# Optimization experiments

Measured on AMD Instinct MI355X. Metric: run time of the kernel, lower is better.

## Reference

```python
import jax, jax.numpy as jnp
import numpy as np

B, S, D, H, V = 32, 1024, 512, 4, 8185
DH = 3 * D // H  # 384 per-head projection; q/k/v each 128
FFN = 4 * D
LN_EPS = 1e-3  # keras LayerNormalization default epsilon


def _pos_encoding(seq_len, d_model):
    pos = np.arange(seq_len)[:, None].astype(np.float32)
    i = np.arange(d_model)[None, :].astype(np.float32)
    angles = pos / np.power(10000.0, 2.0 * (i // 2) / np.float32(d_model))
    angles[:, 0::2] = np.sin(angles[:, 0::2])
    angles[:, 1::2] = np.cos(angles[:, 1::2])
    return jnp.asarray(angles, dtype=jnp.float32)  # [S, D]


def _layernorm(x, g, b):
    mu = jnp.mean(x, axis=-1, keepdims=True)
    var = jnp.mean(jnp.square(x - mu), axis=-1, keepdims=True)
    return (x - mu) * jax.lax.rsqrt(var + LN_EPS) * g + b


def setup_inputs() -> dict:
    key = jax.random.key(0)
    ks = jax.random.split(key, 8)
    sc = 0.02
    return {
        "inputs": jax.random.randint(ks[0], (B, S), 0, V, dtype=jnp.int32),
        "emb": jax.random.normal(ks[1], (V, D), jnp.float32) * sc,
        "Wp": jax.random.normal(ks[2], (H, D, DH), jnp.float32) * sc,
        "bp": jnp.zeros((H, DH), jnp.float32),
        "Wo": jax.random.normal(ks[3], (D, D), jnp.float32) * sc,
        "bo": jnp.zeros((D,), jnp.float32),
        "ln1_g": jnp.ones((D,), jnp.float32),
        "ln1_b": jnp.zeros((D,), jnp.float32),
        "W1": jax.random.normal(ks[4], (D, FFN), jnp.float32) * sc,
        "b1": jnp.zeros((FFN,), jnp.float32),
        "W2": jax.random.normal(ks[5], (FFN, D), jnp.float32) * sc,
        "b2": jnp.zeros((D,), jnp.float32),
        "ln2_g": jnp.ones((D,), jnp.float32),
        "ln2_b": jnp.zeros((D,), jnp.float32),
        "Wh": jax.random.normal(ks[6], (D, D), jnp.float32) * sc,
        "bh": jnp.zeros((D,), jnp.float32),
        "Wf": jax.random.normal(ks[7], (D, 1), jnp.float32) * sc,
        "bf": jnp.zeros((1,), jnp.float32),
    }


def reference(inputs, emb, Wp, bp, Wo, bo, ln1_g, ln1_b, W1, b1, W2, b2,
              ln2_g, ln2_b, Wh, bh, Wf, bf):
    b, s = inputs.shape
    x = emb[inputs] + _pos_encoding(s, emb.shape[1])[None]  # [B,S,D]

    # decoder block: batched per-head projections (q|k|v packed along last axis)
    res = x
    d = jnp.einsum('bsd,hde->bhse', x, Wp) + bp[:, None, :]  # [B,H,S,3*dh]
    q, k, v = jnp.split(d, 3, axis=-1)  # each [B,H,S,dh]
    # NOTE: source scales by rsqrt(seq_len) (tf.shape(k)[1]), not head dim
    scale = jax.lax.rsqrt(jnp.float32(s))
    scores = jnp.einsum('bhse,bhte->bhst', q, k) * scale  # [B,H,S,S]
    heads = jnp.einsum('bhst,bhte->bhse', scores, v)  # linear attn (no softmax)
    concat = heads.transpose(0, 2, 1, 3).reshape(b, s, -1)  # [B,S,D]
    attn = concat @ Wo + bo
    x = _layernorm(attn + res, ln1_g, ln1_b)
    h = jax.nn.relu(x @ W1 + b1) @ W2 + b2
    x = _layernorm(h + x, ln2_g, ln2_b)

    # classification head on first token
    x0 = x[:, 0]
    hid = jax.nn.relu(x0 @ Wh + bh)
    logits = hid @ Wf + bf  # [B,1]
    return logits, jax.nn.sigmoid(logits)
```

## Files before the change

### kernel.cpp

```cpp
#include <hip/hip_runtime.h>
#include <hip/hip_bf16.h>

__global__ __launch_bounds__(256) void qr_k(
    const int* __restrict__ inp, const float* __restrict__ emb,
    const float* __restrict__ Wp, const float* __restrict__ bp,
    float* __restrict__ X0, float* __restrict__ r, float* __restrict__ alpha,
    float* __restrict__ Acc, int* __restrict__ Cnt)
{
    __shared__ float xs[512];
    __shared__ float red[256];
    __shared__ float q0s[128];
    int b = blockIdx.x, h = blockIdx.y, t = threadIdx.x;
    if (b == 0 && h == 0) {
        if (t < 32) Acc[t] = 0.f;
        else if (t < 64) Cnt[t - 32] = 0;
    }
    int tok0 = inp[b * 1024];
#pragma unroll
    for (int rep = 0; rep < 2; rep++) {
        int d = t + rep * 256;
        float v = emb[(long)tok0 * 512 + d] + ((d & 1) ? 1.0f : 0.0f);
        xs[d] = v;
        if (h == 0) X0[b * 512 + d] = v;
    }
    __syncthreads();

    int f = t & 127, dh = t >> 7;
    const float* wq = Wp + (long)h * 196608 + f;
    float acc = 0.f;
#pragma unroll 8
    for (int d = dh * 256; d < dh * 256 + 256; d++)
        acc += xs[d] * wq[(long)d * 384];
    red[t] = acc;
    __syncthreads();
    if (t < 128) q0s[t] = red[t] + red[t + 128] + bp[h * 384 + t];
    __syncthreads();
    if (t < 128) red[t] = q0s[t] * bp[h * 384 + 128 + t];
    __syncthreads();
    for (int w = 64; w >= 1; w >>= 1) {
        if (t < w) red[t] += red[t + w];
        __syncthreads();
    }
    if (t == 0) alpha[b * 4 + h] = red[0];

    const float4* q4 = (const float4*)q0s;
#pragma unroll
    for (int rep = 0; rep < 2; rep++) {
        int d = t + rep * 256;
        const float4* wr = (const float4*)(Wp + ((long)(h * 512 + d)) * 384 + 128);
        float a2 = 0.f;
#pragma unroll 8
        for (int f4 = 0; f4 < 32; f4++) {
            float4 w = wr[f4], qq = q4[f4];
            a2 += w.x * qq.x + w.y * qq.y + w.z * qq.z + w.w * qq.w;
        }
        r[((long)(b * 4 + h)) * 512 + d] = a2;
    }
}

__global__ __launch_bounds__(256) void xu_k(
    const int* __restrict__ inp, const float* __restrict__ emb,
    const float* __restrict__ r, const float* __restrict__ alpha,
    float* __restrict__ Tpp, float* __restrict__ Gp)
{
    __shared__ float redT[4][4][64][8];
    __shared__ float redG[4][4];
    int b = blockIdx.x, sg = blockIdx.y, t = threadIdx.x;
    int wave = t >> 6, lane = t & 63;

    float rsv[4][8];
    float al[4];
#pragma unroll
    for (int h = 0; h < 4; h++) {
        const float4* rp = (const float4*)&r[((long)(b * 4 + h)) * 512 + lane * 8];
        float4 r0 = rp[0], r1 = rp[1];
        rsv[h][0] = r0.x; rsv[h][1] = r0.y; rsv[h][2] = r0.z; rsv[h][3] = r0.w;
        rsv[h][4] = r1.x; rsv[h][5] = r1.y; rsv[h][6] = r1.z; rsv[h][7] = r1.w;
        al[h] = alpha[b * 4 + h];
    }
    float w4[4];
#pragma unroll
    for (int j = 0; j < 4; j++) {
        float expo = (float)(lane * 8 + j * 2) * (1.0f / 512.0f);
        w4[j] = exp2f(-expo * 13.287712379549449f);
    }

    float accT[4][8] = {};
    float gacc[4] = {};
    int s0 = sg * 64 + wave * 16;
#pragma unroll
    for (int g = 0; g < 4; g++) {
        float xv[4][8];
        float up[4][4];
#pragma unroll
        for (int i = 0; i < 4; i++) {
            int srow = s0 + g * 4 + i;
            int tok = inp[b * 1024 + srow];
            const float4* e = (const float4*)&emb[(long)tok * 512 + lane * 8];
            float4 e0 = e[0], e1 = e[1];
            float sf = (float)srow;
            float sv[4], cv[4];
#pragma unroll
            for (int j = 0; j < 4; j++) {
                float ang = sf * w4[j];
                sv[j] = __sinf(ang);
                cv[j] = __cosf(ang);
            }
            xv[i][0] = e0.x + sv[0]; xv[i][1] = e0.y + cv[0];
            xv[i][2] = e0.z + sv[1]; xv[i][3] = e0.w + cv[1];
            xv[i][4] = e1.x + sv[2]; xv[i][5] = e1.y + cv[2];
            xv[i][6] = e1.z + sv[3]; xv[i][7] = e1.w + cv[3];
#pragma unroll
            for (int h = 0; h < 4; h++) {
                float acc = 0.f;
#pragma unroll
                for (int jj = 0; jj < 8; jj++) acc += xv[i][jj] * rsv[h][jj];
                up[i][h] = acc;
            }
        }
#pragma unroll
        for (int off = 32; off; off >>= 1) {
#pragma unroll
            for (int i = 0; i < 4; i++)
#pragma unroll
                for (int h = 0; h < 4; h++)
                    up[i][h] += __shfl_xor(up[i][h], off);
        }
#pragma unroll
        for (int i = 0; i < 4; i++) {
#pragma unroll
            for (int h = 0; h < 4; h++) {
                float u = up[i][h] + al[h];
                gacc[h] += u;
#pragma unroll
                for (int jj = 0; jj < 8; jj++) accT[h][jj] += u * xv[i][jj];
            }
        }
    }
#pragma unroll
    for (int h = 0; h < 4; h++) {
        *(float4*)&redT[wave][h][lane][0] =
            make_float4(accT[h][0], accT[h][1], accT[h][2], accT[h][3]);
        *(float4*)&redT[wave][h][lane][4] =
            make_float4(accT[h][4], accT[h][5], accT[h][6], accT[h][7]);
    }
    if (lane == 0) {
#pragma unroll
        for (int h = 0; h < 4; h++) redG[wave][h] = gacc[h];
    }
    __syncthreads();
    long base = (long)(b * 16 + sg) * 2048;
#pragma unroll
    for (int k = 0; k < 8; k++) {
        int idx = t + k * 256;
        int h = idx >> 9, d = idx & 511;
        float v = redT[0][h][d >> 3][d & 7] + redT[1][h][d >> 3][d & 7]
                + redT[2][h][d >> 3][d & 7] + redT[3][h][d >> 3][d & 7];
        Tpp[base + idx] = v;
    }
    if (t < 4) Gp[(b * 16 + sg) * 4 + t] =
        redG[0][t] + redG[1][t] + redG[2][t] + redG[3][t];
}

__global__ __launch_bounds__(256) void att1_k(
    const float* __restrict__ Tpp, const float* __restrict__ Gp,
    const float* __restrict__ Wp, const float* __restrict__ bp,
    float* __restrict__ C0)
{
    __shared__ float tps[512];
    __shared__ float red[256];
    int b = blockIdx.x, jt = blockIdx.y, t = threadIdx.x;
    int h = jt >> 1, e0 = (jt & 1) * 64;
#pragma unroll
    for (int i = 0; i < 2; i++) {
        int d = t + i * 256;
        float v = 0.f;
#pragma unroll 8
        for (int sg = 0; sg < 16; sg++)
            v += Tpp[(long)b * 32768 + sg * 2048 + h * 512 + d];
        tps[d] = v;
    }
    __syncthreads();
    int e = e0 + (t & 63), rg = t >> 6;
    const float* wv = Wp + (long)h * 196608 + 256 + e;
    float acc = 0.f;
#pragma unroll 8
    for (int d = rg * 128; d < rg * 128 + 128; d++)
        acc += tps[d] * wv[(long)d * 384];
    red[t] = acc;
    __syncthreads();
    if (t < 64) {
        float gam = 0.f;
#pragma unroll
        for (int sg = 0; sg < 16; sg++) gam += Gp[(b * 16 + sg) * 4 + h];
        float sum = red[t] + red[t + 64] + red[t + 128] + red[t + 192];
        float c = 0.03125f * (sum + gam * bp[h * 384 + 256 + e0 + t]);
        C0[b * 512 + h * 128 + e0 + t] = c;
    }
}

__global__ __launch_bounds__(256) void att2s_k(
    const float* __restrict__ C0, const float* __restrict__ Wo,
    const float* __restrict__ bo, const float* __restrict__ X0,
    float* __restrict__ A1, float* __restrict__ Stat)
{
    __shared__ float c0s[512];
    __shared__ float red[256];
    int b = blockIdx.x, jt = blockIdx.y, t = threadIdx.x;
    c0s[t] = C0[b * 512 + t];
    c0s[t + 256] = C0[b * 512 + t + 256];
    __syncthreads();
    int j = jt * 64 + (t & 63), rg = t >> 6;
    float acc = 0.f;
#pragma unroll 8
    for (int d = rg * 128; d < rg * 128 + 128; d++)
        acc += c0s[d] * Wo[(long)d * 512 + j];
    red[t] = acc;
    __syncthreads();
    if (t < 64) {
        int jj = jt * 64 + t;
        float a = red[t] + red[t + 64] + red[t + 128] + red[t + 192]
                + bo[jj] + X0[b * 512 + jj];
        A1[b * 512 + jj] = a;
        float s = a, q = a * a;
#pragma unroll
        for (int off = 32; off; off >>= 1) {
            s += __shfl_down(s, off);
            q += __shfl_down(q, off);
        }
        if (t == 0) {
            Stat[(b * 8 + jt) * 2]     = s;
            Stat[(b * 8 + jt) * 2 + 1] = q;
        }
    }
}

__global__ __launch_bounds__(256) void ffn1_k(
    const float* __restrict__ A1, const float* __restrict__ Stat,
    const float* __restrict__ g1, const float* __restrict__ b1v,
    const float* __restrict__ W1, float* __restrict__ Hp1)
{
    __shared__ float at[32][32];
    __shared__ float mrs[32][2];
    int jt = blockIdx.x, ks = blockIdx.y, t = threadIdx.x;
    if (t < 32) {
        float s = 0.f, q = 0.f;
#pragma unroll
        for (int p8 = 0; p8 < 8; p8++) {
            s += Stat[(t * 8 + p8) * 2];
            q += Stat[(t * 8 + p8) * 2 + 1];
        }
        float mean = s * (1.0f / 512.0f);
        float var = q * (1.0f / 512.0f) - mean * mean;
        mrs[t][0] = mean;
        mrs[t][1] = rsqrtf(var + 0.001f);
    }
    __syncthreads();
    {
        int row = t >> 3, f4 = t & 7;
        int col = ks * 32 + f4 * 4;
        float4 a4 = *(const float4*)&A1[(long)row * 512 + col];
        float4 g4 = *(const float4*)&g1[col];
        float4 bb = *(const float4*)&b1v[col];
        float mean = mrs[row][0], rstd = mrs[row][1];
        float4 v;
        v.x = (a4.x - mean) * rstd * g4.x + bb.x;
        v.y = (a4.y - mean) * rstd * g4.y + bb.y;
        v.z = (a4.z - mean) * rstd * g4.z + bb.z;
        v.w = (a4.w - mean) * rstd * g4.w + bb.w;
        ((float4*)at)[t] = v;
    }
    __syncthreads();
    int j = jt * 64 + (t & 63), rg = t >> 6;
    float acc[8] = {};
    const float* wp = W1 + (long)(ks * 32) * 2048 + j;
#pragma unroll 8
    for (int k = 0; k < 32; k++) {
        float wv = wp[(long)k * 2048];
#pragma unroll
        for (int rr = 0; rr < 8; rr++)
            acc[rr] += at[rg * 8 + rr][k] * wv;
    }
#pragma unroll
    for (int rr = 0; rr < 8; rr++)
        Hp1[((long)(ks * 32 + rg * 8 + rr)) * 2048 + j] = acc[rr];
}

__global__ __launch_bounds__(256) void ffn2_k(
    const float* __restrict__ Hp1, const float* __restrict__ b1,
    const float* __restrict__ W2, float* __restrict__ Hp2)
{
    __shared__ float at[32][32];
    int jt = blockIdx.x, ks2 = blockIdx.y, t = threadIdx.x;
    {
        int row = t >> 3, f4 = t & 7;
        int col4 = ks2 * 8 + f4;
        float4 v = ((const float4*)b1)[col4];
#pragma unroll
        for (int p = 0; p < 16; p++) {
            float4 pv = ((const float4*)Hp1)[(long)p * 16384 + row * 512 + col4];
            v.x += pv.x; v.y += pv.y; v.z += pv.z; v.w += pv.w;
        }
        v.x = fmaxf(v.x, 0.f); v.y = fmaxf(v.y, 0.f);
        v.z = fmaxf(v.z, 0.f); v.w = fmaxf(v.w, 0.f);
        ((float4*)at)[t] = v;
    }
    __syncthreads();
    int j = jt * 64 + (t & 63), rg = t >> 6;
    float acc[8] = {};
    const float* wp = W2 + (long)(ks2 * 32) * 512 + j;
#pragma unroll 8
    for (int k = 0; k < 32; k++) {
        float wv = wp[(long)k * 512];
#pragma unroll
        for (int rr = 0; rr < 8; rr++)
            acc[rr] += at[rg * 8 + rr][k] * wv;
    }
#pragma unroll
    for (int rr = 0; rr < 8; rr++)
        Hp2[((long)(ks2 * 32 + rg * 8 + rr)) * 512 + j] = acc[rr];
}

__global__ __launch_bounds__(256) void headp3_k(
    const float* __restrict__ Hp2, const float* __restrict__ b2,
    const float* __restrict__ A1, const float* __restrict__ Stat,
    const float* __restrict__ g1v, const float* __restrict__ b1v,
    const float* __restrict__ g2v, const float* __restrict__ b2v,
    const float* __restrict__ Wh, const float* __restrict__ bh,
    const float* __restrict__ Wf, const float* __restrict__ bf,
    float* __restrict__ Acc, int* __restrict__ Cnt, float* __restrict__ out)
{
    __shared__ float xs[512];
    __shared__ float red[256];
    __shared__ float sd[8];
    __shared__ float mr[2];
    int b = blockIdx.x, jt = blockIdx.y, t = threadIdx.x;
    if (t == 0) {
        float s = 0.f, q = 0.f;
#pragma unroll
        for (int p8 = 0; p8 < 8; p8++) {
            s += Stat[(b * 8 + p8) * 2];
            q += Stat[(b * 8 + p8) * 2 + 1];
        }
        float mean = s * (1.0f / 512.0f);
        mr[0] = mean;
        mr[1] = rsqrtf(q * (1.0f / 512.0f) - mean * mean + 0.001f);
    }
    __syncthreads();
    float mean1 = mr[0], rstd1 = mr[1];
    float a[2];
#pragma unroll
    for (int rep = 0; rep < 2; rep++) {
        int j = t + rep * 256;
        float y1 = (A1[b * 512 + j] - mean1) * rstd1 * g1v[j] + b1v[j];
        float v = b2[j] + y1;
#pragma unroll 16
        for (int ks = 0; ks < 64; ks++)
            v += Hp2[((long)(ks * 32 + b)) * 512 + j];
        a[rep] = v;
    }
    float s = a[0] + a[1];
#pragma unroll
    for (int off = 32; off; off >>= 1) s += __shfl_down(s, off);
    if ((t & 63) == 0) sd[t >> 6] = s;
    __syncthreads();
    float mean = (sd[0] + sd[1] + sd[2] + sd[3]) * (1.0f / 512.0f);
    float d0 = a[0] - mean, d1 = a[1] - mean;
    float v2 = d0 * d0 + d1 * d1;
#pragma unroll
    for (int off = 32; off; off >>= 1) v2 += __shfl_down(v2, off);
    if ((t & 63) == 0) sd[4 + (t >> 6)] = v2;
    __syncthreads();
    float var = (sd[4] + sd[5] + sd[6] + sd[7]) * (1.0f / 512.0f);
    float rstd = rsqrtf(var + 0.001f);
    xs[t] = d0 * rstd * g2v[t] + b2v[t];
    xs[t + 256] = d1 * rstd * g2v[t + 256] + b2v[t + 256];
    __syncthreads();

    int j = jt * 64 + (t & 63), rg = t >> 6;
    const float* w = Wh + j;
    float acc = 0.f;
#pragma unroll 8
    for (int d = rg * 128; d < rg * 128 + 128; d++)
        acc += xs[d] * w[(long)d * 512];
    red[t] = acc;
    __syncthreads();
    if (t < 64) {
        int jj = jt * 64 + t;
        float hid = red[t] + red[t + 64] + red[t + 128] + red[t + 192] + bh[jj];
        hid = fmaxf(hid, 0.f);
        float p = hid * Wf[jj];
#pragma unroll
        for (int off = 32; off; off >>= 1) p += __shfl_down(p, off);
        if (t == 0) {
            atomicAdd(&Acc[b], p);
            __threadfence();
            int old = atomicAdd(&Cnt[b], 1);
            if (old == 7) {
                float tot = atomicAdd(&Acc[b], 0.0f);
                float logit = tot + bf[0];
                out[b] = logit;
                out[32 + b] = 1.f / (1.f + expf(-logit));
            }
        }
    }
}

extern "C" void kernel_launch(void* const* d_in, const int* in_sizes, int n_in,
                              void* d_out, int out_size, void* d_ws, size_t ws_size,
                              hipStream_t stream)
{
    const int*   inputs = (const int*)  d_in[0];
    const float* emb    = (const float*)d_in[1];
    const float* Wp     = (const float*)d_in[2];
    const float* bp     = (const float*)d_in[3];
    const float* Wo     = (const float*)d_in[4];
    const float* bo     = (const float*)d_in[5];
    const float* ln1_g  = (const float*)d_in[6];
    const float* ln1_b  = (const float*)d_in[7];
    const float* W1     = (const float*)d_in[8];
    const float* b1     = (const float*)d_in[9];
    const float* W2     = (const float*)d_in[10];
    const float* b2     = (const float*)d_in[11];
    const float* ln2_g  = (const float*)d_in[12];
    const float* ln2_b  = (const float*)d_in[13];
    const float* Wh     = (const float*)d_in[14];
    const float* bh     = (const float*)d_in[15];
    const float* Wf     = (const float*)d_in[16];
    const float* bf     = (const float*)d_in[17];
    float* out = (float*)d_out;

    char* p = (char*)d_ws;
    float* X0    = (float*)p;  p += 65536;
    float* r     = (float*)p;  p += 262144;
    float* alpha = (float*)p;  p += 1024;
    float* Gp    = (float*)p;  p += 8192;
    float* Tpp   = (float*)p;  p += 4194304;
    float* C0    = (float*)p;  p += 65536;
    float* A1    = (float*)p;  p += 65536;
    float* Stat  = (float*)p;  p += 2048;
    float* Acc   = (float*)p;  p += 512;
    int*   Cnt   = (int*)p;    p += 512;
    float* Hp1   = (float*)p;  p += 4194304;
    float* Hp2   = (float*)p;  p += 4194304;

    qr_k<<<dim3(32, 4), 256, 0, stream>>>(inputs, emb, Wp, bp, X0, r, alpha,
                                          Acc, Cnt);
    xu_k<<<dim3(32, 16), 256, 0, stream>>>(inputs, emb, r, alpha, Tpp, Gp);
    att1_k<<<dim3(32, 8), 256, 0, stream>>>(Tpp, Gp, Wp, bp, C0);
    att2s_k<<<dim3(32, 8), 256, 0, stream>>>(C0, Wo, bo, X0, A1, Stat);
    ffn1_k<<<dim3(32, 16), 256, 0, stream>>>(A1, Stat, ln1_g, ln1_b, W1, Hp1);
    ffn2_k<<<dim3(8, 64), 256, 0, stream>>>(Hp1, b1, W2, Hp2);
    headp3_k<<<dim3(32, 8), 256, 0, stream>>>(Hp2, b2, A1, Stat,
                                              ln1_g, ln1_b, ln2_g, ln2_b,
                                              Wh, bh, Wf, bf, Acc, Cnt, out);
}
```

Baseline: 187.0 us.

## Fuse seven stage kernels into one persistent kernel with global atomic barriers

Replaces the chain of seven kernel launches with a single grid-stride persistent kernel of 512 blocks. Stages are separated by a software grid barrier built on atomic counters, and a small init kernel resets the counters. The aim is to remove per-launch gaps and tail effects between the small dependent stages. The barrier spins on atomics and assumes all 512 blocks are co-resident (launch bounds 256,2), so it risks deadlock if they are not, and it adds polling overhead.

```diff
diff --git a/kernel.cpp b/kernel.cpp
--- a/kernel.cpp
+++ b/kernel.cpp
@@ -1,406 +1,429 @@
 #include <hip/hip_runtime.h>
 #include <hip/hip_bf16.h>
 
-__global__ __launch_bounds__(256) void qr_k(
+__device__ __forceinline__ void gbar(int* __restrict__ bar, int nblk)
+{
+    __syncthreads();
+    __threadfence();
+    if (threadIdx.x == 0) {
+        atomicAdd(bar, 1);
+        while (atomicAdd(bar, 0) < nblk)
+            __builtin_amdgcn_s_sleep(1);
+    }
+    __syncthreads();
+    __threadfence();
+}
+
+__global__ __launch_bounds__(64) void init_k(
+    float* __restrict__ Acc, int* __restrict__ Cnt, int* __restrict__ Bar)
+{
+    int t = threadIdx.x;
+    if (t < 32) { Acc[t] = 0.f; Cnt[t] = 0; }
+    if (t < 8)  Bar[t] = 0;
+}
+
+__global__ __launch_bounds__(256, 2) void mega_k(
     const int* __restrict__ inp, const float* __restrict__ emb,
     const float* __restrict__ Wp, const float* __restrict__ bp,
-    float* __restrict__ X0, float* __restrict__ r, float* __restrict__ alpha,
-    float* __restrict__ Acc, int* __restrict__ Cnt)
-{
-    __shared__ float xs[512];
-    __shared__ float red[256];
-    __shared__ float q0s[128];
-    int b = blockIdx.x, h = blockIdx.y, t = threadIdx.x;
-    if (b == 0 && h == 0) {
-        if (t < 32) Acc[t] = 0.f;
-        else if (t < 64) Cnt[t - 32] = 0;
-    }
-    int tok0 = inp[b * 1024];
-#pragma unroll
-    for (int rep = 0; rep < 2; rep++) {
-        int d = t + rep * 256;
-        float v = emb[(long)tok0 * 512 + d] + ((d & 1) ? 1.0f : 0.0f);
-        xs[d] = v;
-        if (h == 0) X0[b * 512 + d] = v;
-    }
-    __syncthreads();
-
-    int f = t & 127, dh = t >> 7;
-    const float* wq = Wp + (long)h * 196608 + f;
-    float acc = 0.f;
-#pragma unroll 8
-    for (int d = dh * 256; d < dh * 256 + 256; d++)
-        acc += xs[d] * wq[(long)d * 384];
-    red[t] = acc;
-    __syncthreads();
-    if (t < 128) q0s[t] = red[t] + red[t + 128] + bp[h * 384 + t];
-    __syncthreads();
-    if (t < 128) red[t] = q0s[t] * bp[h * 384 + 128 + t];
-    __syncthreads();
-    for (int w = 64; w >= 1; w >>= 1) {
-        if (t < w) red[t] += red[t + w];
-        __syncthreads();
-    }
-    if (t == 0) alpha[b * 4 + h] = red[0];
-
-    const float4* q4 = (const float4*)q0s;
-#pragma unroll
-    for (int rep = 0; rep < 2; rep++) {
-        int d = t + rep * 256;
-        const float4* wr = (const float4*)(Wp + ((long)(h * 512 + d)) * 384 + 128);
-        float a2 = 0.f;
-#pragma unroll 8
-        for (int f4 = 0; f4 < 32; f4++) {
-            float4 w = wr[f4], qq = q4[f4];
-            a2 += w.x * qq.x + w.y * qq.y + w.z * qq.z + w.w * qq.w;
-        }
-        r[((long)(b * 4 + h)) * 512 + d] = a2;
-    }
-}
-
-__global__ __launch_bounds__(256) void xu_k(
-    const int* __restrict__ inp, const float* __restrict__ emb,
-    const float* __restrict__ r, const float* __restrict__ alpha,
-    float* __restrict__ Tpp, float* __restrict__ Gp)
-{
-    __shared__ float redT[4][4][64][8];
-    __shared__ float redG[4][4];
-    int b = blockIdx.x, sg = blockIdx.y, t = threadIdx.x;
-    int wave = t >> 6, lane = t & 63;
-
-    float rsv[4][8];
-    float al[4];
-#pragma unroll
-    for (int h = 0; h < 4; h++) {
-        const float4* rp = (const float4*)&r[((long)(b * 4 + h)) * 512 + lane * 8];
-        float4 r0 = rp[0], r1 = rp[1];
-        rsv[h][0] = r0.x; rsv[h][1] = r0.y; rsv[h][2] = r0.z; rsv[h][3] = r0.w;
-        rsv[h][4] = r1.x; rsv[h][5] = r1.y; rsv[h][6] = r1.z; rsv[h][7] = r1.w;
-        al[h] = alpha[b * 4 + h];
-    }
-    float w4[4];
-#pragma unroll
-    for (int j = 0; j < 4; j++) {
-        float expo = (float)(lane * 8 + j * 2) * (1.0f / 512.0f);
-        w4[j] = exp2f(-expo * 13.287712379549449f);
-    }
-
-    float accT[4][8] = {};
-    float gacc[4] = {};
-    int s0 = sg * 64 + wave * 16;
-#pragma unroll
-    for (int g = 0; g < 4; g++) {
-        float xv[4][8];
-        float up[4][4];
-#pragma unroll
-        for (int i = 0; i < 4; i++) {
-            int srow = s0 + g * 4 + i;
-            int tok = inp[b * 1024 + srow];
-            const float4* e = (const float4*)&emb[(long)tok * 512 + lane * 8];
-            float4 e0 = e[0], e1 = e[1];
-            float sf = (float)srow;
-            float sv[4], cv[4];
-#pragma unroll
-            for (int j = 0; j < 4; j++) {
-                float ang = sf * w4[j];
-                sv[j] = __sinf(ang);
-                cv[j] = __cosf(ang);
-            }
-            xv[i][0] = e0.x + sv[0]; xv[i][1] = e0.y + cv[0];
-            xv[i][2] = e0.z + sv[1]; xv[i][3] = e0.w + cv[1];
-            xv[i][4] = e1.x + sv[2]; xv[i][5] = e1.y + cv[2];
-            xv[i][6] = e1.z + sv[3]; xv[i][7] = e1.w + cv[3];
-#pragma unroll
-            for (int h = 0; h < 4; h++) {
-                float acc = 0.f;
-#pragma unroll
-                for (int jj = 0; jj < 8; jj++) acc += xv[i][jj] * rsv[h][jj];
-                up[i][h] = acc;
-            }
-        }
-#pragma unroll
-        for (int off = 32; off; off >>= 1) {
-#pragma unroll
-            for (int i = 0; i < 4; i++)
-#pragma unroll
-                for (int h = 0; h < 4; h++)
-                    up[i][h] += __shfl_xor(up[i][h], off);
-        }
-#pragma unroll
-        for (int i = 0; i < 4; i++) {
-#pragma unroll
-            for (int h = 0; h < 4; h++) {
-                float u = up[i][h] + al[h];
-                gacc[h] += u;
-#pragma unroll
-                for (int jj = 0; jj < 8; jj++) accT[h][jj] += u * xv[i][jj];
-            }
-        }
-    }
-#pragma unroll
-    for (int h = 0; h < 4; h++) {
-        *(float4*)&redT[wave][h][lane][0] =
-            make_float4(accT[h][0], accT[h][1], accT[h][2], accT[h][3]);
-        *(float4*)&redT[wave][h][lane][4] =
-            make_float4(accT[h][4], accT[h][5], accT[h][6], accT[h][7]);
-    }
-    if (lane == 0) {
-#pragma unroll
-        for (int h = 0; h < 4; h++) redG[wave][h] = gacc[h];
-    }
-    __syncthreads();
-    long base = (long)(b * 16 + sg) * 2048;
-#pragma unroll
-    for (int k = 0; k < 8; k++) {
-        int idx = t + k * 256;
-        int h = idx >> 9, d = idx & 511;
-        float v = redT[0][h][d >> 3][d & 7] + redT[1][h][d >> 3][d & 7]
-                + redT[2][h][d >> 3][d & 7] + redT[3][h][d >> 3][d & 7];
-        Tpp[base + idx] = v;
-    }
-    if (t < 4) Gp[(b * 16 + sg) * 4 + t] =
-        redG[0][t] + redG[1][t] + redG[2][t] + redG[3][t];
-}
-
-__global__ __launch_bounds__(256) void att1_k(
-    const float* __restrict__ Tpp, const float* __restrict__ Gp,
-    const float* __restrict__ Wp, const float* __restrict__ bp,
-    float* __restrict__ C0)
-{
-    __shared__ float tps[512];
-    __shared__ float red[256];
-    int b = blockIdx.x, jt = blockIdx.y, t = threadIdx.x;
-    int h = jt >> 1, e0 = (jt & 1) * 64;
-#pragma unroll
-    for (int i = 0; i < 2; i++) {
-        int d = t + i * 256;
-        float v = 0.f;
-#pragma unroll 8
-        for (int sg = 0; sg < 16; sg++)
-            v += Tpp[(long)b * 32768 + sg * 2048 + h * 512 + d];
-        tps[d] = v;
-    }
-    __syncthreads();
-    int e = e0 + (t & 63), rg = t >> 6;
-    const float* wv = Wp + (long)h * 196608 + 256 + e;
-    float acc = 0.f;
-#pragma unroll 8
-    for (int d = rg * 128; d < rg * 128 + 128; d++)
-        acc += tps[d] * wv[(long)d * 384];
-    red[t] = acc;
-    __syncthreads();
-    if (t < 64) {
-        float gam = 0.f;
-#pragma unroll
-        for (int sg = 0; sg < 16; sg++) gam += Gp[(b * 16 + sg) * 4 + h];
-        float sum = red[t] + red[t + 64] + red[t + 128] + red[t + 192];
-        float c = 0.03125f * (sum + gam * bp[h * 384 + 256 + e0 + t]);
-        C0[b * 512 + h * 128 + e0 + t] = c;
-    }
-}
-
-__global__ __launch_bounds__(256) void att2s_k(
-    const float* __restrict__ C0, const float* __restrict__ Wo,
-    const float* __restrict__ bo, const float* __restrict__ X0,
-    float* __restrict__ A1, float* __restrict__ Stat)
-{
-    __shared__ float c0s[512];
-    __shared__ float red[256];
-    int b = blockIdx.x, jt = blockIdx.y, t = threadIdx.x;
-    c0s[t] = C0[b * 512 + t];
-    c0s[t + 256] = C0[b * 512 + t + 256];
-    __syncthreads();
-    int j = jt * 64 + (t & 63), rg = t >> 6;
-    float acc = 0.f;
-#pragma unroll 8
-    for (int d = rg * 128; d < rg * 128 + 128; d++)
-        acc += c0s[d] * Wo[(long)d * 512 + j];
-    red[t] = acc;
-    __syncthreads();
-    if (t < 64) {
-        int jj = jt * 64 + t;
-        float a = red[t] + red[t + 64] + red[t + 128] + red[t + 192]
-                + bo[jj] + X0[b * 512 + jj];
-        A1[b * 512 + jj] = a;
-        float s = a, q = a * a;
-#pragma unroll
-        for (int off = 32; off; off >>= 1) {
-            s += __shfl_down(s, off);
-            q += __shfl_down(q, off);
-        }
-        if (t == 0) {
-            Stat[(b * 8 + jt) * 2]     = s;
-            Stat[(b * 8 + jt) * 2 + 1] = q;
-        }
-    }
-}
-
-__global__ __launch_bounds__(256) void ffn1_k(
-    const float* __restrict__ A1, const float* __restrict__ Stat,
-    const float* __restrict__ g1, const float* __restrict__ b1v,
-    const float* __restrict__ W1, float* __restrict__ Hp1)
-{
-    __shared__ float at[32][32];
-    __shared__ float mrs[32][2];
-    int jt = blockIdx.x, ks = blockIdx.y, t = threadIdx.x;
-    if (t < 32) {
-        float s = 0.f, q = 0.f;
-#pragma unroll
-        for (int p8 = 0; p8 < 8; p8++) {
-            s += Stat[(t * 8 + p8) * 2];
-            q += Stat[(t * 8 + p8) * 2 + 1];
-        }
-        float mean = s * (1.0f / 512.0f);
-        float var = q * (1.0f / 512.0f) - mean * mean;
-        mrs[t][0] = mean;
-        mrs[t][1] = rsqrtf(var + 0.001f);
-    }
-    __syncthreads();
-    {
-        int row = t >> 3, f4 = t & 7;
-        int col = ks * 32 + f4 * 4;
-        float4 a4 = *(const float4*)&A1[(long)row * 512 + col];
-        float4 g4 = *(const float4*)&g1[col];
-        float4 bb = *(const float4*)&b1v[col];
-        float mean = mrs[row][0], rstd = mrs[row][1];
-        float4 v;
-        v.x = (a4.x - mean) * rstd * g4.x + bb.x;
-        v.y = (a4.y - mean) * rstd * g4.y + bb.y;
-        v.z = (a4.z - mean) * rstd * g4.z + bb.z;
-        v.w = (a4.w - mean) * rstd * g4.w + bb.w;
-        ((float4*)at)[t] = v;
-    }
-    __syncthreads();
-    int j = jt * 64 + (t & 63), rg = t >> 6;
-    float acc[8] = {};
-    const float* wp = W1 + (long)(ks * 32) * 2048 + j;
-#pragma unroll 8
-    for (int k = 0; k < 32; k++) {
-        float wv = wp[(long)k * 2048];
-#pragma unroll
-        for (int rr = 0; rr < 8; rr++)
-            acc[rr] += at[rg * 8 + rr][k] * wv;
-    }
-#pragma unroll
-    for (int rr = 0; rr < 8; rr++)
-        Hp1[((long)(ks * 32 + rg * 8 + rr)) * 2048 + j] = acc[rr];
-}
-
-__global__ __launch_bounds__(256) void ffn2_k(
-    const float* __restrict__ Hp1, const float* __restrict__ b1,
-    const float* __restrict__ W2, float* __restrict__ Hp2)
-{
-    __shared__ float at[32][32];
-    int jt = blockIdx.x, ks2 = blockIdx.y, t = threadIdx.x;
-    {
-        int row = t >> 3, f4 = t & 7;
-        int col4 = ks2 * 8 + f4;
-        float4 v = ((const float4*)b1)[col4];
-#pragma unroll
-        for (int p = 0; p < 16; p++) {
-            float4 pv = ((const float4*)Hp1)[(long)p * 16384 + row * 512 + col4];
-            v.x += pv.x; v.y += pv.y; v.z += pv.z; v.w += pv.w;
-        }
-        v.x = fmaxf(v.x, 0.f); v.y = fmaxf(v.y, 0.f);
-        v.z = fmaxf(v.z, 0.f); v.w = fmaxf(v.w, 0.f);
-        ((float4*)at)[t] = v;
-    }
-    __syncthreads();
-    int j = jt * 64 + (t & 63), rg = t >> 6;
-    float acc[8] = {};
-    const float* wp = W2 + (long)(ks2 * 32) * 512 + j;
-#pragma unroll 8
-    for (int k = 0; k < 32; k++) {
-        float wv = wp[(long)k * 512];
-#pragma unroll
-        for (int rr = 0; rr < 8; rr++)
-            acc[rr] += at[rg * 8 + rr][k] * wv;
-    }
-#pragma unroll
-    for (int rr = 0; rr < 8; rr++)
-        Hp2[((long)(ks2 * 32 + rg * 8 + rr)) * 512 + j] = acc[rr];
-}
-
-__global__ __launch_bounds__(256) void headp3_k(
-    const float* __restrict__ Hp2, const float* __restrict__ b2,
-    const float* __restrict__ A1, const float* __restrict__ Stat,
+    const float* __restrict__ Wo, const float* __restrict__ bo,
     const float* __restrict__ g1v, const float* __restrict__ b1v,
+    const float* __restrict__ W1, const float* __restrict__ b1,
+    const float* __restrict__ W2, const float* __restrict__ b2,
     const float* __restrict__ g2v, const float* __restrict__ b2v,
     const float* __restrict__ Wh, const float* __restrict__ bh,
     const float* __restrict__ Wf, const float* __restrict__ bf,
-    float* __restrict__ Acc, int* __restrict__ Cnt, float* __restrict__ out)
+    float* __restrict__ X0, float* __restrict__ r, float* __restrict__ alpha,
+    float* __restrict__ Gp, float* __restrict__ Tpp, float* __restrict__ C0,
+    float* __restrict__ A1, float* __restrict__ Stat, float* __restrict__ Acc,
+    int* __restrict__ Cnt, float* __restrict__ Hp1, float* __restrict__ Hp2,
+    int* __restrict__ Bar, float* __restrict__ out)
 {
-    __shared__ float xs[512];
-    __shared__ float red[256];
-    __shared__ float sd[8];
-    __shared__ float mr[2];
-    int b = blockIdx.x, jt = blockIdx.y, t = threadIdx.x;
-    if (t == 0) {
-        float s = 0.f, q = 0.f;
-#pragma unroll
-        for (int p8 = 0; p8 < 8; p8++) {
-            s += Stat[(b * 8 + p8) * 2];
-            q += Stat[(b * 8 + p8) * 2 + 1];
-        }
-        float mean = s * (1.0f / 512.0f);
-        mr[0] = mean;
-        mr[1] = rsqrtf(q * (1.0f / 512.0f) - mean * mean + 0.001f);
-    }
-    __syncthreads();
-    float mean1 = mr[0], rstd1 = mr[1];
-    float a[2];
-#pragma unroll
-    for (int rep = 0; rep < 2; rep++) {
-        int j = t + rep * 256;
-        float y1 = (A1[b * 512 + j] - mean1) * rstd1 * g1v[j] + b1v[j];
-        float v = b2[j] + y1;
+    __shared__ __align__(16) float sm[8224];
+    int t = threadIdx.x;
+    int blk = blockIdx.x, gsz = gridDim.x;
+    int wave = t >> 6, lane = t & 63;
+
+    {
+        float* xs = sm;
+        float* red = sm + 512;
+        float* q0s = sm + 768;
+        for (int tk = blk; tk < 256; tk += gsz) {
+            __syncthreads();
+            int b = tk >> 3, h = (tk >> 1) & 3, rh = tk & 1;
+            int tok0 = inp[b * 1024];
+#pragma unroll
+            for (int rep = 0; rep < 2; rep++) {
+                int d = t + rep * 256;
+                float v = emb[(long)tok0 * 512 + d] + ((d & 1) ? 1.0f : 0.0f);
+                xs[d] = v;
+                if (h == 0 && rh == 0) X0[b * 512 + d] = v;
+            }
+            __syncthreads();
+            int f = t & 127, dh = t >> 7;
+            const float* wq = Wp + (long)h * 196608 + f;
+            float acc = 0.f;
+#pragma unroll 8
+            for (int d = dh * 256; d < dh * 256 + 256; d++)
+                acc += xs[d] * wq[(long)d * 384];
+            red[t] = acc;
+            __syncthreads();
+            if (t < 128) q0s[t] = red[t] + red[t + 128] + bp[h * 384 + t];
+            __syncthreads();
+            if (t < 128) red[t] = q0s[t] * bp[h * 384 + 128 + t];
+            __syncthreads();
+            for (int w = 64; w >= 1; w >>= 1) {
+                if (t < w) red[t] += red[t + w];
+                __syncthreads();
+            }
+            if (t == 0 && rh == 0) alpha[b * 4 + h] = red[0];
+            const float4* q4 = (const float4*)q0s;
+            int d = t + rh * 256;
+            const float4* wr = (const float4*)(Wp + ((long)(h * 512 + d)) * 384 + 128);
+            float a2 = 0.f;
+#pragma unroll 8
+            for (int f4 = 0; f4 < 32; f4++) {
+                float4 w = wr[f4], qq = q4[f4];
+                a2 += w.x * qq.x + w.y * qq.y + w.z * qq.z + w.w * qq.w;
+            }
+            r[((long)(b * 4 + h)) * 512 + d] = a2;
+        }
+    }
+    gbar(&Bar[0], gsz);
+
+    {
+        float* redT = sm;
+        float* redG = sm + 8192;
+        float w4[4];
+#pragma unroll
+        for (int j = 0; j < 4; j++) {
+            float expo = (float)(lane * 8 + j * 2) * (1.0f / 512.0f);
+            w4[j] = exp2f(-expo * 13.287712379549449f);
+        }
+        for (int tk = blk; tk < 512; tk += gsz) {
+            __syncthreads();
+            int b = tk >> 4, sg = tk & 15;
+            float rsv[4][8], al[4];
+#pragma unroll
+            for (int h = 0; h < 4; h++) {
+                const float4* rp = (const float4*)&r[((long)(b * 4 + h)) * 512 + lane * 8];
+                float4 r0 = rp[0], r1 = rp[1];
+                rsv[h][0] = r0.x; rsv[h][1] = r0.y; rsv[h][2] = r0.z; rsv[h][3] = r0.w;
+                rsv[h][4] = r1.x; rsv[h][5] = r1.y; rsv[h][6] = r1.z; rsv[h][7] = r1.w;
+                al[h] = alpha[b * 4 + h];
+            }
+            float accT[4][8] = {};
+            float gacc[4] = {};
+            int s0 = sg * 64 + wave * 16;
+#pragma unroll
+            for (int g = 0; g < 4; g++) {
+                float xv[4][8];
+                float up[4][4];
+#pragma unroll
+                for (int i = 0; i < 4; i++) {
+                    int srow = s0 + g * 4 + i;
+                    int tok = inp[b * 1024 + srow];
+                    const float4* e = (const float4*)&emb[(long)tok * 512 + lane * 8];
+                    float4 e0 = e[0], e1 = e[1];
+                    float sf = (float)srow;
+                    float sv[4], cv[4];
+#pragma unroll
+                    for (int j = 0; j < 4; j++) {
+                        float ang = sf * w4[j];
+                        sv[j] = __sinf(ang);
+                        cv[j] = __cosf(ang);
+                    }
+                    xv[i][0] = e0.x + sv[0]; xv[i][1] = e0.y + cv[0];
+                    xv[i][2] = e0.z + sv[1]; xv[i][3] = e0.w + cv[1];
+                    xv[i][4] = e1.x + sv[2]; xv[i][5] = e1.y + cv[2];
+                    xv[i][6] = e1.z + sv[3]; xv[i][7] = e1.w + cv[3];
+#pragma unroll
+                    for (int h = 0; h < 4; h++) {
+                        float acc = 0.f;
+#pragma unroll
+                        for (int jj = 0; jj < 8; jj++) acc += xv[i][jj] * rsv[h][jj];
+                        up[i][h] = acc;
+                    }
+                }
+#pragma unroll
+                for (int off = 32; off; off >>= 1) {
+#pragma unroll
+                    for (int i = 0; i < 4; i++)
+#pragma unroll
+                        for (int h = 0; h < 4; h++)
+                            up[i][h] += __shfl_xor(up[i][h], off);
+                }
+#pragma unroll
+                for (int i = 0; i < 4; i++) {
+#pragma unroll
+                    for (int h = 0; h < 4; h++) {
+                        float u = up[i][h] + al[h];
+                        gacc[h] += u;
+#pragma unroll
+                        for (int jj = 0; jj < 8; jj++) accT[h][jj] += u * xv[i][jj];
+                    }
+                }
+            }
+#pragma unroll
+            for (int h = 0; h < 4; h++) {
+                *(float4*)&redT[wave * 2048 + h * 512 + lane * 8] =
+                    make_float4(accT[h][0], accT[h][1], accT[h][2], accT[h][3]);
+                *(float4*)&redT[wave * 2048 + h * 512 + lane * 8 + 4] =
+                    make_float4(accT[h][4], accT[h][5], accT[h][6], accT[h][7]);
+            }
+            if (lane == 0) {
+#pragma unroll
+                for (int h = 0; h < 4; h++) redG[wave * 4 + h] = gacc[h];
+            }
+            __syncthreads();
+            long base = (long)(b * 16 + sg) * 2048;
+#pragma unroll
+            for (int k = 0; k < 8; k++) {
+                int idx = t + k * 256;
+                float v = redT[idx] + redT[2048 + idx]
+                        + redT[4096 + idx] + redT[6144 + idx];
+                Tpp[base + idx] = v;
+            }
+            if (t < 4) Gp[(b * 16 + sg) * 4 + t] =
+                redG[t] + redG[4 + t] + redG[8 + t] + redG[12 + t];
+        }
+    }
+    gbar(&Bar[1], gsz);
+
+    {
+        float* tps = sm;
+        float* red = sm + 512;
+        for (int tk = blk; tk < 256; tk += gsz) {
+            __syncthreads();
+            int b = tk >> 3, jt = tk & 7;
+            int h = jt >> 1, e0 = (jt & 1) * 64;
+#pragma unroll
+            for (int i = 0; i < 2; i++) {
+                int d = t + i * 256;
+                float v = 0.f;
+#pragma unroll 8
+                for (int sg = 0; sg < 16; sg++)
+                    v += Tpp[(long)b * 32768 + sg * 2048 + h * 512 + d];
+                tps[d] = v;
+            }
+            __syncthreads();
+            int e = e0 + (t & 63), rg = t >> 6;
+            const float* wv = Wp + (long)h * 196608 + 256 + e;
+            float acc = 0.f;
+#pragma unroll 8
+            for (int d = rg * 128; d < rg * 128 + 128; d++)
+                acc += tps[d] * wv[(long)d * 384];
+            red[t] = acc;
+            __syncthreads();
+            if (t < 64) {
+                float gam = 0.f;
+#pragma unroll
+                for (int sg = 0; sg < 16; sg++) gam += Gp[(b * 16 + sg) * 4 + h];
+                float sum = red[t] + red[t + 64] + red[t + 128] + red[t + 192];
+                float c = 0.03125f * (sum + gam * bp[h * 384 + 256 + e0 + t]);
+                C0[b * 512 + h * 128 + e0 + t] = c;
+            }
+        }
+    }
+    gbar(&Bar[2], gsz);
+
+    {
+        float* c0s = sm;
+        float* red = sm + 512;
+        for (int tk = blk; tk < 256; tk += gsz) {
+            __syncthreads();
+            int b = tk >> 3, jt = tk & 7;
+            c0s[t] = C0[b * 512 + t];
+            c0s[t + 256] = C0[b * 512 + t + 256];
+            __syncthreads();
+            int j = jt * 64 + (t & 63), rg = t >> 6;
+            float acc = 0.f;
+#pragma unroll 8
+            for (int d = rg * 128; d < rg * 128 + 128; d++)
+                acc += c0s[d] * Wo[(long)d * 512 + j];
+            red[t] = acc;
+            __syncthreads();
+            if (t < 64) {
+                int jj = jt * 64 + t;
+                float a = red[t] + red[t + 64] + red[t + 128] + red[t + 192]
+                        + bo[jj] + X0[b * 512 + jj];
+                A1[b * 512 + jj] = a;
+                float s = a, q = a * a;
+#pragma unroll
+                for (int off = 32; off; off >>= 1) {
+                    s += __shfl_down(s, off);
+                    q += __shfl_down(q, off);
+                }
+                if (t == 0) {
+                    Stat[(b * 8 + jt) * 2]     = s;
+                    Stat[(b * 8 + jt) * 2 + 1] = q;
+                }
+            }
+        }
+    }
+    gbar(&Bar[3], gsz);
+
+    {
+        float* at = sm;
+        float* mrs = sm + 1024;
+        for (int tk = blk; tk < 512; tk += gsz) {
+            __syncthreads();
+            int jt = tk & 31, ks = tk >> 5;
+            if (t < 32) {
+                float s = 0.f, q = 0.f;
+#pragma unroll
+                for (int p8 = 0; p8 < 8; p8++) {
+                    s += Stat[(t * 8 + p8) * 2];
+                    q += Stat[(t * 8 + p8) * 2 + 1];
+                }
+                float mean = s * (1.0f / 512.0f);
+                float var = q * (1.0f / 512.0f) - mean * mean;
+                mrs[t * 2] = mean;
+                mrs[t * 2 + 1] = rsqrtf(var + 0.001f);
+            }
+            __syncthreads();
+            {
+                int row = t >> 3, f4 = t & 7;
+                int col = ks * 32 + f4 * 4;
+                float4 a4 = *(const float4*)&A1[(long)row * 512 + col];
+                float4 g4 = *(const float4*)&g1v[col];
+                float4 bb = *(const float4*)&b1v[col];
+                float mean = mrs[row * 2], rstd = mrs[row * 2 + 1];
+                float4 v;
+                v.x = (a4.x - mean) * rstd * g4.x + bb.x;
+                v.y = (a4.y - mean) * rstd * g4.y + bb.y;
+                v.z = (a4.z - mean) * rstd * g4.z + bb.z;
+                v.w = (a4.w - mean) * rstd * g4.w + bb.w;
+                ((float4*)at)[t] = v;
+            }
+            __syncthreads();
+            int j = jt * 64 + (t & 63), rg = t >> 6;
+            float acc[8] = {};
+            const float* wp = W1 + (long)(ks * 32) * 2048 + j;
+#pragma unroll 8
+            for (int k = 0; k < 32; k++) {
+                float wv = wp[(long)k * 2048];
+#pragma unroll
+                for (int rr = 0; rr < 8; rr++)
+                    acc[rr] += at[(rg * 8 + rr) * 32 + k] * wv;
+            }
+#pragma unroll
+            for (int rr = 0; rr < 8; rr++)
+                Hp1[((long)(ks * 32 + rg * 8 + rr)) * 2048 + j] = acc[rr];
+        }
+    }
+    gbar(&Bar[4], gsz);
+
+    {
+        float* at = sm;
+        for (int tk = blk; tk < 512; tk += gsz) {
+            __syncthreads();
+            int jt = tk & 7, ks2 = tk >> 3;
+            {
+                int row = t >> 3, f4 = t & 7;
+                int col4 = ks2 * 8 + f4;
+                float4 v = ((const float4*)b1)[col4];
+#pragma unroll
+                for (int p = 0; p < 16; p++) {
+                    float4 pv = ((const float4*)Hp1)[(long)p * 16384 + row * 512 + col4];
+                    v.x += pv.x; v.y += pv.y; v.z += pv.z; v.w += pv.w;
+                }
+                v.x = fmaxf(v.x, 0.f); v.y = fmaxf(v.y, 0.f);
+                v.z = fmaxf(v.z, 0.f); v.w = fmaxf(v.w, 0.f);
+                ((float4*)at)[t] = v;
+            }
+            __syncthreads();
+            int j = jt * 64 + (t & 63), rg = t >> 6;
+            float acc[8] = {};
+            const float* wp = W2 + (long)(ks2 * 32) * 512 + j;
+#pragma unroll 8
+            for (int k = 0; k < 32; k++) {
+                float wv = wp[(long)k * 512];
+#pragma unroll
+                for (int rr = 0; rr < 8; rr++)
+                    acc[rr] += at[(rg * 8 + rr) * 32 + k] * wv;
+            }
+#pragma unroll
+            for (int rr = 0; rr < 8; rr++)
+                Hp2[((long)(ks2 * 32 + rg * 8 + rr)) * 512 + j] = acc[rr];
+        }
+    }
+    gbar(&Bar[5], gsz);
+
+    {
+        float* xs = sm;
+        float* red = sm + 512;
+        float* sd = sm + 768;
+        float* mr = sm + 776;
+        for (int tk = blk; tk < 256; tk += gsz) {
+            __syncthreads();
+            int b = tk >> 3, jt = tk & 7;
+            if (t == 0) {
+                float s = 0.f, q = 0.f;
+#pragma unroll
+                for (int p8 = 0; p8 < 8; p8++) {
+                    s += Stat[(b * 8 + p8) * 2];
+                    q += Stat[(b * 8 + p8) * 2 + 1];
+                }
+                float mean = s * (1.0f / 512.0f);
+                mr[0] = mean;
+                mr[1] = rsqrtf(q * (1.0f / 512.0f) - mean * mean + 0.001f);
+            }
+            __syncthreads();
+            float mean1 = mr[0], rstd1 = mr[1];
+            float a[2];
+#pragma unroll
+            for (int rep = 0; rep < 2; rep++) {
+                int j = t + rep * 256;
+                float y1 = (A1[b * 512 + j] - mean1) * rstd1 * g1v[j] + b1v[j];
+                float v = b2[j] + y1;
 #pragma unroll 16
-        for (int ks = 0; ks < 64; ks++)
-            v += Hp2[((long)(ks * 32 + b)) * 512 + j];
-        a[rep] = v;
-    }
-    float s = a[0] + a[1];
-#pragma unroll
-    for (int off = 32; off; off >>= 1) s += __shfl_down(s, off);
-    if ((t & 63) == 0) sd[t >> 6] = s;
-    __syncthreads();
-    float mean = (sd[0] + sd[1] + sd[2] + sd[3]) * (1.0f / 512.0f);
-    float d0 = a[0] - mean, d1 = a[1] - mean;
-    float v2 = d0 * d0 + d1 * d1;
-#pragma unroll
-    for (int off = 32; off; off >>= 1) v2 += __shfl_down(v2, off);
-    if ((t & 63) == 0) sd[4 + (t >> 6)] = v2;
-    __syncthreads();
-    float var = (sd[4] + sd[5] + sd[6] + sd[7]) * (1.0f / 512.0f);
-    float rstd = rsqrtf(var + 0.001f);
-    xs[t] = d0 * rstd * g2v[t] + b2v[t];
-    xs[t + 256] = d1 * rstd * g2v[t + 256] + b2v[t + 256];
-    __syncthreads();
-
-    int j = jt * 64 + (t & 63), rg = t >> 6;
-    const float* w = Wh + j;
-    float acc = 0.f;
-#pragma unroll 8
-    for (int d = rg * 128; d < rg * 128 + 128; d++)
-        acc += xs[d] * w[(long)d * 512];
-    red[t] = acc;
-    __syncthreads();
-    if (t < 64) {
-        int jj = jt * 64 + t;
-        float hid = red[t] + red[t + 64] + red[t + 128] + red[t + 192] + bh[jj];
-        hid = fmaxf(hid, 0.f);
-        float p = hid * Wf[jj];
-#pragma unroll
-        for (int off = 32; off; off >>= 1) p += __shfl_down(p, off);
-        if (t == 0) {
-            atomicAdd(&Acc[b], p);
-            __threadfence();
-            int old = atomicAdd(&Cnt[b], 1);
-            if (old == 7) {
-                float tot = atomicAdd(&Acc[b], 0.0f);
-                float logit = tot + bf[0];
-                out[b] = logit;
-                out[32 + b] = 1.f / (1.f + expf(-logit));
+                for (int ks = 0; ks < 64; ks++)
+                    v += Hp2[((long)(ks * 32 + b)) * 512 + j];
+                a[rep] = v;
+            }
+            float s = a[0] + a[1];
+#pragma unroll
+            for (int off = 32; off; off >>= 1) s += __shfl_down(s, off);
+            if ((t & 63) == 0) sd[t >> 6] = s;
+            __syncthreads();
+            float mean = (sd[0] + sd[1] + sd[2] + sd[3]) * (1.0f / 512.0f);
+            float d0 = a[0] - mean, d1 = a[1] - mean;
+            float v2 = d0 * d0 + d1 * d1;
+#pragma unroll
+            for (int off = 32; off; off >>= 1) v2 += __shfl_down(v2, off);
+            if ((t & 63) == 0) sd[4 + (t >> 6)] = v2;
+            __syncthreads();
+            float var = (sd[4] + sd[5] + sd[6] + sd[7]) * (1.0f / 512.0f);
+            float rstd = rsqrtf(var + 0.001f);
+            xs[t] = d0 * rstd * g2v[t] + b2v[t];
+            xs[t + 256] = d1 * rstd * g2v[t + 256] + b2v[t + 256];
+            __syncthreads();
+            int j = jt * 64 + (t & 63), rg = t >> 6;
+            const float* w = Wh + j;
+            float acc = 0.f;
+#pragma unroll 8
+            for (int d = rg * 128; d < rg * 128 + 128; d++)
+                acc += xs[d] * w[(long)d * 512];
+            red[t] = acc;
+            __syncthreads();
+            if (t < 64) {
+                int jj = jt * 64 + t;
+                float hid = red[t] + red[t + 64] + red[t + 128] + red[t + 192] + bh[jj];
+                hid = fmaxf(hid, 0.f);
+                float p = hid * Wf[jj];
+#pragma unroll
+                for (int off = 32; off; off >>= 1) p += __shfl_down(p, off);
+                if (t == 0) {
+                    atomicAdd(&Acc[b], p);
+                    __threadfence();
+                    int old = atomicAdd(&Cnt[b], 1);
+                    if (old == 7) {
+                        float tot = atomicAdd(&Acc[b], 0.0f);
+                        float logit = tot + bf[0];
+                        out[b] = logit;
+                        out[32 + b] = 1.f / (1.f + expf(-logit));
+                    }
+                }
             }
         }
     }
@@ -441,17 +464,13 @@
     float* Stat  = (float*)p;  p += 2048;
     float* Acc   = (float*)p;  p += 512;
     int*   Cnt   = (int*)p;    p += 512;
+    int*   Bar   = (int*)p;    p += 512;
     float* Hp1   = (float*)p;  p += 4194304;
     float* Hp2   = (float*)p;  p += 4194304;
 
-    qr_k<<<dim3(32, 4), 256, 0, stream>>>(inputs, emb, Wp, bp, X0, r, alpha,
-                                          Acc, Cnt);
-    xu_k<<<dim3(32, 16), 256, 0, stream>>>(inputs, emb, r, alpha, Tpp, Gp);
-    att1_k<<<dim3(32, 8), 256, 0, stream>>>(Tpp, Gp, Wp, bp, C0);
-    att2s_k<<<dim3(32, 8), 256, 0, stream>>>(C0, Wo, bo, X0, A1, Stat);
-    ffn1_k<<<dim3(32, 16), 256, 0, stream>>>(A1, Stat, ln1_g, ln1_b, W1, Hp1);
-    ffn2_k<<<dim3(8, 64), 256, 0, stream>>>(Hp1, b1, W2, Hp2);
-    headp3_k<<<dim3(32, 8), 256, 0, stream>>>(Hp2, b2, A1, Stat,
-                                              ln1_g, ln1_b, ln2_g, ln2_b,
-                                              Wh, bh, Wf, bf, Acc, Cnt, out);
+    init_k<<<dim3(1), 64, 0, stream>>>(Acc, Cnt, Bar);
+    mega_k<<<dim3(512), 256, 0, stream>>>(
+        inputs, emb, Wp, bp, Wo, bo, ln1_g, ln1_b, W1, b1, W2, b2,
+        ln2_g, ln2_b, Wh, bh, Wf, bf,
+        X0, r, alpha, Gp, Tpp, C0, A1, Stat, Acc, Cnt, Hp1, Hp2, Bar, out);
 }
```

New measurement: 709.5 us. 3.79x slower.
